# Kernel optimization log

Hardware: AMD Instinct MI355X
Metric: run time of the kernel (lower is better)

Reference implementation:

```python
import jax, jax.numpy as jnp
import numpy as np

D_MODEL = 1024
EXPAND = 2
D_INNER = EXPAND * D_MODEL      # 2048
D_STATE = 2
D_CONV = 4
DT_RANK = (D_MODEL + 15) // 16  # 64
BATCH, SEQ = 2, 4096
LN_EPS = 1e-5


def setup_inputs() -> dict:
    key = jax.random.key(0)
    ks = jax.random.split(key, 16)
    s = 0.02
    inp = {
        "x":       jax.random.normal(ks[0], (BATCH, SEQ, D_MODEL), jnp.float32),
        # Mamba params (torch Linear convention: W is [out, in])
        "w_in":    jax.random.normal(ks[1], (2 * D_INNER, D_MODEL), jnp.float32) * s,
        "conv_w":  jax.random.normal(ks[2], (D_INNER, 1, D_CONV), jnp.float32) * s,
        "conv_b":  jnp.zeros((D_INNER,), jnp.float32),
        "w_xproj": jax.random.normal(ks[3], (DT_RANK + 2 * D_STATE, D_INNER), jnp.float32) * s,
        "w_dt":    jax.random.normal(ks[4], (D_INNER, DT_RANK), jnp.float32) * s,
        "b_dt":    jax.random.normal(ks[5], (D_INNER,), jnp.float32) * s - 4.0,  # softplus -> small dt
        "a_log":   jnp.log(jnp.broadcast_to(jnp.arange(1, D_STATE + 1, dtype=jnp.float32), (D_INNER, D_STATE))),
        "d_skip":  jnp.ones((D_INNER,), jnp.float32),
        "w_out":   jax.random.normal(ks[6], (D_MODEL, D_INNER), jnp.float32) * s,
        # LayerNorms
        "ln1_g":   jnp.ones((D_MODEL,), jnp.float32),
        "ln1_b":   jnp.zeros((D_MODEL,), jnp.float32),
        "ln2_g":   jnp.ones((D_MODEL,), jnp.float32),
        "ln2_b":   jnp.zeros((D_MODEL,), jnp.float32),
        # FFN (Linear d->d, ReLU, Linear d->d; dropout inactive at eval)
        "ffn_w1":  jax.random.normal(ks[7], (D_MODEL, D_MODEL), jnp.float32) * s,
        "ffn_b1":  jnp.zeros((D_MODEL,), jnp.float32),
        "ffn_w2":  jax.random.normal(ks[8], (D_MODEL, D_MODEL), jnp.float32) * s,
        "ffn_b2":  jnp.zeros((D_MODEL,), jnp.float32),
    }
    return inp


def _ln(x, g, b):
    mu = x.mean(-1, keepdims=True)
    v = ((x - mu) ** 2).mean(-1, keepdims=True)
    return (x - mu) * jax.lax.rsqrt(v + LN_EPS) * g + b


def _mamba(x, w_in, conv_w, conv_b, w_xproj, w_dt, b_dt, a_log, d_skip, w_out):
    Bsz = x.shape[0]
    xz = x @ w_in.T                      # (B,L,2*D_INNER)
    xp, z = jnp.split(xz, 2, axis=-1)
    # depthwise causal conv over time
    xc = jnp.transpose(xp, (0, 2, 1))    # (B,D,L)
    xc = jax.lax.conv_general_dilated(
        xc, conv_w, window_strides=(1,), padding=[(D_CONV - 1, 0)],
        feature_group_count=D_INNER)
    xc = xc + conv_b[None, :, None]
    xp = jax.nn.silu(jnp.transpose(xc, (0, 2, 1)))   # (B,L,D)
    # input-dependent SSM params
    x_dbl = xp @ w_xproj.T               # (B,L,DT_RANK+2N)
    dt, Bm, Cm = jnp.split(x_dbl, [DT_RANK, DT_RANK + D_STATE], axis=-1)
    dt = jax.nn.softplus(dt @ w_dt.T + b_dt)          # (B,L,D)
    A = -jnp.exp(a_log)                  # (D,N)
    dA = jnp.exp(dt[..., None] * A)                  # (B,L,D,N)
    dBu = dt[..., None] * Bm[:, :, None, :] * xp[..., None]  # (B,L,D,N)

    def step(h, inp):
        da, dbu, c = inp                 # (B,D,N),(B,D,N),(B,N)
        h = da * h + dbu
        y = jnp.einsum('bdn,bn->bd', h, c)
        return h, y

    h0 = jnp.zeros((Bsz, D_INNER, D_STATE), x.dtype)
    _, ys = jax.lax.scan(step, h0, (jnp.swapaxes(dA, 0, 1),
                                    jnp.swapaxes(dBu, 0, 1),
                                    jnp.swapaxes(Cm, 0, 1)))
    y = jnp.swapaxes(ys, 0, 1)           # (B,L,D)
    y = (y + d_skip * xp) * jax.nn.silu(z)
    return y @ w_out.T                   # (B,L,d_model)


def reference(x, w_in, conv_w, conv_b, w_xproj, w_dt, b_dt, a_log, d_skip, w_out,
              ln1_g, ln1_b, ln2_g, ln2_b, ffn_w1, ffn_b1, ffn_w2, ffn_b2):
    h = x + _mamba(_ln(x, ln1_g, ln1_b), w_in, conv_w, conv_b, w_xproj,
                   w_dt, b_dt, a_log, d_skip, w_out)
    f = _ln(h, ln2_g, ln2_b)
    f = jax.nn.relu(f @ ffn_w1.T + ffn_b1) @ ffn_w2.T + ffn_b2
    return h + f
```

## Files before the change

kernel.cpp:

```cpp
#include <hip/hip_runtime.h>

typedef unsigned short u16;
typedef __bf16 bf16x8 __attribute__((ext_vector_type(8)));
typedef float f32x4 __attribute__((ext_vector_type(4)));
typedef float f32x2 __attribute__((ext_vector_type(2)));
typedef u16 u16x4 __attribute__((ext_vector_type(4)));
typedef u16 u16x8 __attribute__((ext_vector_type(8)));

#define SEQ   4096
#define DM    1024
#define DI    2048
#define NTOK  8192
#define NXP   68
#define DTR   64
#define NCH   4096
#define CHUNK 32
#define NCHK  128

__device__ __forceinline__ float bf2f(u16 v) {
  union { unsigned u; float f; } x; x.u = ((unsigned)v) << 16; return x.f;
}
__device__ __forceinline__ u16 f2bf(float f) {
  unsigned u = __float_as_uint(f);
  return (u16)((u + 0x7FFFu + ((u >> 16) & 1u)) >> 16);
}

__device__ __forceinline__ void g2l16(const u16* g, u16* l) {
  __builtin_amdgcn_global_load_lds(
      (const __attribute__((address_space(1))) unsigned int*)g,
      (__attribute__((address_space(3))) unsigned int*)l, 16, 0, 0);
}

#define SBAR0() __builtin_amdgcn_sched_barrier(0)

__global__ __launch_bounds__(256)
void detect_kernel(const u16* __restrict__ x, int* __restrict__ flag)
{
  __shared__ int tot;
  if (threadIdx.x == 0) tot = 0;
  __syncthreads();
  int cnt = 0;
  for (int i = threadIdx.x; i < 4096; i += 256) {
    const int e = (x[2 * i] >> 7) & 0xFF;
    if (e > 167) cnt++;
  }
  atomicAdd(&tot, cnt);
  __syncthreads();
  if (threadIdx.x == 0) flag[0] = (tot >= 8) ? 1 : 0;
}

#define NW0 4194304
#define NW1  139264
#define NW2  131072
#define NW3 2097152
#define NW4 1048576
#define NW5 1048576
#define NBB 4228
__global__ __launch_bounds__(256)
void convert_all(const float* __restrict__ s0, const float* __restrict__ s1,
                 const float* __restrict__ s2, const float* __restrict__ s3,
                 const float* __restrict__ s4, const float* __restrict__ s5,
                 u16* __restrict__ d0, u16* __restrict__ d1, u16* __restrict__ d2,
                 u16* __restrict__ d3, u16* __restrict__ d4, u16* __restrict__ d5,
                 const void* t0, const void* t1, const void* t2, const void* t3,
                 const void* t4, const void* t5, const void* t6, const void* t7,
                 const void* t8, const void* t9, const void* t10,
                 u16* __restrict__ dsm, const int* __restrict__ flag)
{
  if (blockIdx.x >= NBB) {
    const int i = (blockIdx.x - NBB) * 256 + threadIdx.x;
    if (i >= 24576) return;
    const void* src; int off; int dsti = i;
    if      (i < 8192)  { src = t0;  off = i;
                          dsti = (off & 3) * DI + (off >> 2); }
    else if (i < 10240) { src = t1;  off = i - 8192; }
    else if (i < 12288) { src = t2;  off = i - 10240; }
    else if (i < 16384) { src = t3;  off = i - 12288; }
    else if (i < 18432) { src = t4;  off = i - 16384; }
    else if (i < 19456) { src = t5;  off = i - 18432; }
    else if (i < 20480) { src = t6;  off = i - 19456; }
    else if (i < 21504) { src = t7;  off = i - 20480; }
    else if (i < 22528) { src = t8;  off = i - 21504; }
    else if (i < 23552) { src = t9;  off = i - 22528; }
    else                { src = t10; off = i - 23552; }
    dsm[dsti] = (*flag) ? f2bf(((const float*)src)[off]) : ((const u16*)src)[off];
    return;
  }
  if (*flag == 0) return;
  long e = ((long)blockIdx.x * 256 + threadIdx.x) * 8;
  const long c1 = NW0, c2 = c1 + NW1, c3 = c2 + NW2, c4 = c3 + NW3,
             c5 = c4 + NW4, c6 = c5 + NW5;
  if (e >= c6) return;
  const float* s; u16* d;
  if      (e < c1) { s = s0;          d = d0; }
  else if (e < c2) { s = s1; e -= c1; d = d1; }
  else if (e < c3) { s = s2; e -= c2; d = d2; }
  else if (e < c4) { s = s3; e -= c3; d = d3; }
  else if (e < c5) { s = s4; e -= c4; d = d4; }
  else             { s = s5; e -= c5; d = d5; }
  f32x4 a = *(const f32x4*)(s + e);
  f32x4 b = *(const f32x4*)(s + e + 4);
  u16x8 o;
#pragma unroll
  for (int k = 0; k < 4; ++k) { o[k] = f2bf(a[k]); o[4 + k] = f2bf(b[k]); }
  *(u16x8*)(d + e) = o;
}

template<int MODE>
__global__ __launch_bounds__(256)
void ln_kernel(const void* __restrict__ xin, const u16* __restrict__ gw,
               const u16* __restrict__ bw, u16* __restrict__ outp,
               const int* __restrict__ flag)
{
  const int tid = threadIdx.x;
  const int sub = tid >> 7;
  const int col0 = (tid & 127) * 8;
  const int row = blockIdx.x * 2 + sub;
  const bool isf32 = (MODE == 0) ? (*flag != 0) : false;
  float v[8];
  if (isf32) {
    const float* xf = (const float*)xin + (size_t)row * DM + col0;
    f32x4 a = *(const f32x4*)xf, b2 = *(const f32x4*)(xf + 4);
#pragma unroll
    for (int k = 0; k < 4; ++k) { v[k] = a[k]; v[4 + k] = b2[k]; }
  } else {
    u16x8 xb = *(const u16x8*)((const u16*)xin + (size_t)row * DM + col0);
#pragma unroll
    for (int k = 0; k < 8; ++k) v[k] = bf2f(xb[k]);
  }
  float s = 0.f, s2 = 0.f;
#pragma unroll
  for (int k = 0; k < 8; ++k) { s += v[k]; s2 += v[k] * v[k]; }
#pragma unroll
  for (int off = 32; off > 0; off >>= 1) {
    s  += __shfl_down(s,  off);
    s2 += __shfl_down(s2, off);
  }
  __shared__ float red[4], red2[4];
  __shared__ f32x2 stat[2];
  const int wv = tid >> 6;
  if ((tid & 63) == 0) { red[wv] = s; red2[wv] = s2; }
  __syncthreads();
  if ((tid & 127) == 0) {
    float ts = red[sub * 2] + red[sub * 2 + 1];
    float t2 = red2[sub * 2] + red2[sub * 2 + 1];
    float mu = ts * (1.f / DM);
    float var = t2 * (1.f / DM) - mu * mu;
    stat[sub] = f32x2{mu, rsqrtf(var + 1e-5f)};
  }
  __syncthreads();
  const float mu = stat[sub][0], rs = stat[sub][1];
  u16x8 gv = *(const u16x8*)(gw + col0), bv = *(const u16x8*)(bw + col0);
  u16x8 o;
#pragma unroll
  for (int k = 0; k < 8; ++k)
    o[k] = f2bf((v[k] - mu) * rs * bf2f(gv[k]) + bf2f(bv[k]));
  *(u16x8*)(outp + (size_t)row * DM + col0) = o;
}

template<int EPI, int LNBX>
__global__ __launch_bounds__(256, 2)
void gemm_kernel(const u16* __restrict__ A, const u16* __restrict__ Bc,
                 const u16* __restrict__ Braw,
                 int M, int N, int K,
                 const u16* __restrict__ bias, const u16* __restrict__ addbf,
                 const float* __restrict__ addf, const int* __restrict__ dtflag,
                 void* __restrict__ Cp, void* __restrict__ Cp2)
{
  __shared__ __align__(16) u16 sA[2][128 * 32];
  __shared__ __align__(16) u16 sB[2][128 * 32];
  const int fl = *dtflag;
  const u16* __restrict__ B = fl ? Bc : Braw;
  const int tid = threadIdx.x;
  const int b = blockIdx.x;
  const int xcd = b & 7;
  const int kk = b >> 3;
  const int bx = kk & ((1 << LNBX) - 1);
  const int by = xcd * 8 + (kk >> LNBX);
  const int m0 = by * 128;
  const int n0 = bx * 128;
  const int lane = tid & 63;
  const int wv = tid >> 6;
  const int wm = (wv & 1) * 64;
  const int wn = (wv >> 1) * 64;
  const int r = lane & 15;
  const int q = lane >> 4;
  const int rsw = (r >> 1) & 3;

  const int pr = lane >> 2;
  const int kc = (lane & 3) ^ ((pr >> 1) & 3);
  const int pk = kc * 8;
  u16* lA0[2] = { &sA[0][(wv * 2 + 0) * 512], &sA[1][(wv * 2 + 0) * 512] };
  u16* lA1[2] = { &sA[0][(wv * 2 + 1) * 512], &sA[1][(wv * 2 + 1) * 512] };
  u16* lB0[2] = { &sB[0][(wv * 2 + 0) * 512], &sB[1][(wv * 2 + 0) * 512] };
  u16* lB1[2] = { &sB[0][(wv * 2 + 1) * 512], &sB[1][(wv * 2 + 1) * 512] };
  const u16* gA0 = A + (size_t)(m0 + wv * 32 + pr) * K + pk;
  const u16* gA1 = gA0 + (size_t)16 * K;
  const u16* gB0 = B + (size_t)(n0 + wv * 32 + pr) * K + pk;
  const u16* gB1 = gB0 + (size_t)16 * K;

  f32x4 acc[4][4];
#pragma unroll
  for (int i = 0; i < 4; ++i)
#pragma unroll
    for (int j = 0; j < 4; ++j)
#pragma unroll
      for (int t = 0; t < 4; ++t) acc[i][j][t] = 0.f;

  g2l16(gA0, lA0[0]); g2l16(gA1, lA1[0]);
  g2l16(gB0, lB0[0]); g2l16(gB1, lB1[0]);

  const int nk = K >> 5;
  for (int kt = 0; kt < nk; ++kt) {
    const int cur = kt & 1;
    __syncthreads();
    bf16x8 af[4], bfr[4];
#pragma unroll
    for (int i = 0; i < 4; ++i)
      af[i] = *reinterpret_cast<const bf16x8*>(
          &sA[cur][(wm + i * 16 + r) * 32 + (q ^ rsw) * 8]);
#pragma unroll
    for (int j = 0; j < 4; ++j)
      bfr[j] = *reinterpret_cast<const bf16x8*>(
          &sB[cur][(wn + j * 16 + r) * 32 + (q ^ rsw) * 8]);
    if (kt + 1 < nk) {
      gA0 += 32; gA1 += 32; gB0 += 32; gB1 += 32;
      g2l16(gA0, lA0[cur ^ 1]); g2l16(gA1, lA1[cur ^ 1]);
      g2l16(gB0, lB0[cur ^ 1]); g2l16(gB1, lB1[cur ^ 1]);
    }
#pragma unroll
    for (int i = 0; i < 4; ++i)
#pragma unroll
      for (int j = 0; j < 4; ++j)
        acc[i][j] = __builtin_amdgcn_mfma_f32_16x16x32_bf16(af[i], bfr[j], acc[i][j], 0, 0, 0);
  }

  __syncthreads();
  float* ep = (wv < 2) ? ((float*)&sA[0][0] + wv * 2048)
                       : ((float*)&sB[0][0] + (wv - 2) * 2048);
  const int r2 = lane >> 2;
  const int ccol = ((lane & 3) ^ (r2 & 3)) * 16;

#pragma unroll
  for (int i = 0; i < 4; ++i) {
#pragma unroll
    for (int j = 0; j < 4; ++j)
#pragma unroll
      for (int t = 0; t < 4; ++t)
        ep[(q * 4 + t) * 68 + j * 16 + r] = acc[i][j][t];
    f32x4 w0 = *(const f32x4*)&ep[r2 * 68 + ccol + 0];
    f32x4 w1 = *(const f32x4*)&ep[r2 * 68 + ccol + 4];
    f32x4 w2 = *(const f32x4*)&ep[r2 * 68 + ccol + 8];
    f32x4 w3 = *(const f32x4*)&ep[r2 * 68 + ccol + 12];
    float vv[16];
#pragma unroll
    for (int k = 0; k < 4; ++k) {
      vv[k] = w0[k]; vv[4 + k] = w1[k]; vv[8 + k] = w2[k]; vv[12 + k] = w3[k];
    }
    const int row = m0 + wm + i * 16 + r2;
    const int colg = n0 + wn + ccol;
    const size_t idx = (size_t)row * N + colg;
    if (EPI == 2) {
      u16x8 b0 = *(const u16x8*)&bias[colg];
      u16x8 b1 = *(const u16x8*)&bias[colg + 8];
      u16x8 o0, o1;
#pragma unroll
      for (int k = 0; k < 8; ++k) {
        float v0 = vv[k] + bf2f(b0[k]);
        float v1 = vv[8 + k] + bf2f(b1[k]);
        v0 = (v0 > 15.f) ? v0 : __logf(1.f + __expf(v0));
        v1 = (v1 > 15.f) ? v1 : __logf(1.f + __expf(v1));
        o0[k] = f2bf(v0); o1[k] = f2bf(v1);
      }
      *(u16x8*)&((u16*)Cp)[idx] = o0;
      *(u16x8*)&((u16*)Cp)[idx + 8] = o1;
    } else if (EPI == 3) {
      float ax[16];
      if (fl) {
        f32x4 a0 = *(const f32x4*)&addf[idx];
        f32x4 a1 = *(const f32x4*)&addf[idx + 4];
        f32x4 a2 = *(const f32x4*)&addf[idx + 8];
        f32x4 a3 = *(const f32x4*)&addf[idx + 12];
#pragma unroll
        for (int k = 0; k < 4; ++k) {
          ax[k] = a0[k]; ax[4 + k] = a1[k]; ax[8 + k] = a2[k]; ax[12 + k] = a3[k];
        }
      } else {
        u16x8 a0 = *(const u16x8*)&addbf[idx];
        u16x8 a1 = *(const u16x8*)&addbf[idx + 8];
#pragma unroll
        for (int k = 0; k < 8; ++k) { ax[k] = bf2f(a0[k]); ax[8 + k] = bf2f(a1[k]); }
      }
      u16x8 o0, o1;
#pragma unroll
      for (int k = 0; k < 8; ++k) {
        o0[k] = f2bf(vv[k] + ax[k]); o1[k] = f2bf(vv[8 + k] + ax[8 + k]);
      }
      *(u16x8*)&((u16*)Cp)[idx] = o0;
      *(u16x8*)&((u16*)Cp)[idx + 8] = o1;
    } else if (EPI == 4) {
      u16x8 b0 = *(const u16x8*)&bias[colg];
      u16x8 b1 = *(const u16x8*)&bias[colg + 8];
      u16x8 o0, o1;
#pragma unroll
      for (int k = 0; k < 8; ++k) {
        o0[k] = f2bf(fmaxf(vv[k] + bf2f(b0[k]), 0.f));
        o1[k] = f2bf(fmaxf(vv[8 + k] + bf2f(b1[k]), 0.f));
      }
      *(u16x8*)&((u16*)Cp)[idx] = o0;
      *(u16x8*)&((u16*)Cp)[idx + 8] = o1;
    } else {
      u16x8 b0 = *(const u16x8*)&bias[colg];
      u16x8 b1 = *(const u16x8*)&bias[colg + 8];
      u16x8 a0 = *(const u16x8*)&addbf[idx];
      u16x8 a1 = *(const u16x8*)&addbf[idx + 8];
      float r0[8], r1[8];
#pragma unroll
      for (int k = 0; k < 8; ++k) {
        r0[k] = vv[k] + bf2f(b0[k]) + bf2f(a0[k]);
        r1[k] = vv[8 + k] + bf2f(b1[k]) + bf2f(a1[k]);
      }
      if (fl) {
        f32x4 f0, f1, f2, f3;
#pragma unroll
        for (int k = 0; k < 4; ++k) { f0[k] = r0[k]; f1[k] = r0[4 + k]; f2[k] = r1[k]; f3[k] = r1[4 + k]; }
        *(f32x4*)&((float*)Cp)[idx] = f0;
        *(f32x4*)&((float*)Cp)[idx + 4] = f1;
        *(f32x4*)&((float*)Cp)[idx + 8] = f2;
        *(f32x4*)&((float*)Cp)[idx + 12] = f3;
      } else {
        u16x8 o0, o1;
#pragma unroll
        for (int k = 0; k < 8; ++k) { o0[k] = f2bf(r0[k]); o1[k] = f2bf(r1[k]); }
        *(u16x8*)&((u16*)Cp)[idx] = o0;
        *(u16x8*)&((u16*)Cp)[idx + 8] = o1;
      }
    }
  }
}

template<int EPI, int LNBX>
__global__ __launch_bounds__(512, 2)
void gemm256_kernel(const u16* __restrict__ A, const u16* __restrict__ Bc,
                    const u16* __restrict__ Braw, int M, int N, int K,
                    const int* __restrict__ dtflag, void* __restrict__ Cp,
                    void* __restrict__ Cp2)
{
  __shared__ __align__(16) u16 sAB[2][2][2][128 * 64];
  (void)M;
  const int fl = *dtflag;
  const u16* __restrict__ B = fl ? Bc : Braw;
  const int tid = threadIdx.x;
  const int w = tid >> 6;
  const int lane = tid & 63;
  const int b = blockIdx.x;
  const int wg = (b & 7) * (gridDim.x >> 3) + (b >> 3);
  const int bx = wg & ((1 << LNBX) - 1);
  const int by = wg >> LNBX;
  const int m0 = by * 256;
  const int n0 = bx * 256;
  const int wm = w >> 2;
  const int wn = w & 3;
  const int r = lane & 15;
  const int q = lane >> 4;
  const int r7 = r & 7;
  const int srow = lane >> 3;
  const int schunk = ((lane & 7) ^ (srow & 7)) << 3;

  auto stageA = [&](int buf, int half, int kt) {
#pragma unroll
    for (int j = 0; j < 2; ++j) {
      u16* l = &sAB[buf][0][half][(w * 16 + j * 8) * 64];
      const u16* g = A + (size_t)(m0 + half * 128 + w * 16 + j * 8 + srow) * K
                       + (kt << 6) + schunk;
      g2l16(g, l);
    }
  };
  auto stageB = [&](int buf, int half, int kt) {
#pragma unroll
    for (int j = 0; j < 2; ++j) {
      u16* l = &sAB[buf][1][half][(w * 16 + j * 8) * 64];
      const u16* g = B + (size_t)(n0 + half * 128 + w * 16 + j * 8 + srow) * K
                       + (kt << 6) + schunk;
      g2l16(g, l);
    }
  };

  f32x4 acc[8][4];
#pragma unroll
  for (int i = 0; i < 8; ++i)
#pragma unroll
    for (int j = 0; j < 4; ++j)
#pragma unroll
      for (int t = 0; t < 4; ++t) acc[i][j][t] = 0.f;

  const int nk = K >> 6;
  stageA(0, 0, 0); stageA(0, 1, 0); stageB(0, 0, 0); stageB(0, 1, 0);
  if (nk > 1) { stageB(1, 0, 1); stageB(1, 1, 1); }
  if (nk > 1) asm volatile("s_waitcnt vmcnt(4)" ::: "memory");
  else        asm volatile("s_waitcnt vmcnt(0)" ::: "memory");
  SBAR0();
  __builtin_amdgcn_s_barrier();
  SBAR0();

  for (int kt = 0; kt < nk; ++kt) {
    const int c = kt & 1;
    const u16* bA = &sAB[c][0][wm][0];
    const u16* bB = &sAB[c][1][wn >> 1][0];
    const int rB = (wn & 1) * 64;
    bf16x8 af03[4][2], af47[4][2], b01[2][2], b23[2][2];

#pragma unroll
    for (int mf = 0; mf < 4; ++mf)
#pragma unroll
      for (int ks = 0; ks < 2; ++ks)
        af03[mf][ks] = *(const bf16x8*)&bA[(mf * 16 + r) * 64
                          + ((((ks << 2) + q) ^ r7) << 3)];
#pragma unroll
    for (int nf = 0; nf < 2; ++nf)
#pragma unroll
      for (int ks = 0; ks < 2; ++ks)
        b01[nf][ks] = *(const bf16x8*)&bB[(rB + nf * 16 + r) * 64
                          + ((((ks << 2) + q) ^ r7) << 3)];
    if (kt + 1 < nk) stageA(c ^ 1, 0, kt + 1);
    SBAR0(); __builtin_amdgcn_s_barrier();
    asm volatile("s_waitcnt lgkmcnt(0)" ::: "memory"); SBAR0();
    __builtin_amdgcn_s_setprio(1);
#pragma unroll
    for (int mf = 0; mf < 4; ++mf)
#pragma unroll
      for (int nf = 0; nf < 2; ++nf)
#pragma unroll
        for (int ks = 0; ks < 2; ++ks)
          acc[mf][nf] = __builtin_amdgcn_mfma_f32_16x16x32_bf16(
              af03[mf][ks], b01[nf][ks], acc[mf][nf], 0, 0, 0);
    __builtin_amdgcn_s_setprio(0);
    SBAR0(); __builtin_amdgcn_s_barrier(); SBAR0();

#pragma unroll
    for (int nf = 0; nf < 2; ++nf)
#pragma unroll
      for (int ks = 0; ks < 2; ++ks)
        b23[nf][ks] = *(const bf16x8*)&bB[(rB + (nf + 2) * 16 + r) * 64
                          + ((((ks << 2) + q) ^ r7) << 3)];
    if (kt + 1 < nk) stageA(c ^ 1, 1, kt + 1);
    SBAR0(); __builtin_amdgcn_s_barrier();
    asm volatile("s_waitcnt lgkmcnt(0)" ::: "memory"); SBAR0();
    __builtin_amdgcn_s_setprio(1);
#pragma unroll
    for (int mf = 0; mf < 4; ++mf)
#pragma unroll
      for (int nf = 0; nf < 2; ++nf)
#pragma unroll
        for (int ks = 0; ks < 2; ++ks)
          acc[mf][nf + 2] = __builtin_amdgcn_mfma_f32_16x16x32_bf16(
              af03[mf][ks], b23[nf][ks], acc[mf][nf + 2], 0, 0, 0);
    __builtin_amdgcn_s_setprio(0);
    SBAR0(); __builtin_amdgcn_s_barrier(); SBAR0();

#pragma unroll
    for (int mf = 0; mf < 4; ++mf)
#pragma unroll
      for (int ks = 0; ks < 2; ++ks)
        af47[mf][ks] = *(const bf16x8*)&bA[((mf + 4) * 16 + r) * 64
                          + ((((ks << 2) + q) ^ r7) << 3)];
    if (kt + 2 < nk) stageB(c, 0, kt + 2);
    SBAR0(); __builtin_amdgcn_s_barrier();
    asm volatile("s_waitcnt lgkmcnt(0)" ::: "memory"); SBAR0();
    __builtin_amdgcn_s_setprio(1);
#pragma unroll
    for (int mf = 0; mf < 4; ++mf)
#pragma unroll
      for (int nf = 0; nf < 2; ++nf)
#pragma unroll
        for (int ks = 0; ks < 2; ++ks)
          acc[mf + 4][nf + 2] = __builtin_amdgcn_mfma_f32_16x16x32_bf16(
              af47[mf][ks], b23[nf][ks], acc[mf + 4][nf + 2], 0, 0, 0);
    __builtin_amdgcn_s_setprio(0);
    SBAR0(); __builtin_amdgcn_s_barrier(); SBAR0();

    if (kt + 2 < nk) stageB(c, 1, kt + 2);
    SBAR0(); __builtin_amdgcn_s_barrier(); SBAR0();
    __builtin_amdgcn_s_setprio(1);
#pragma unroll
    for (int mf = 0; mf < 4; ++mf)
#pragma unroll
      for (int nf = 0; nf < 2; ++nf)
#pragma unroll
        for (int ks = 0; ks < 2; ++ks)
          acc[mf + 4][nf] = __builtin_amdgcn_mfma_f32_16x16x32_bf16(
              af47[mf][ks], b01[nf][ks], acc[mf + 4][nf], 0, 0, 0);
    __builtin_amdgcn_s_setprio(0);
    SBAR0();
    if (kt + 2 < nk) asm volatile("s_waitcnt vmcnt(4)" ::: "memory");
    else             asm volatile("s_waitcnt vmcnt(0)" ::: "memory");
    SBAR0();
    __builtin_amdgcn_s_barrier();
    SBAR0();
  }

  float* ep = (float*)&sAB[0][0][0][0] + w * 4096;
  const int r2 = lane >> 2;
  const int ccol = ((lane & 3) ^ (r2 & 3)) * 16;
  u16* C6 = (n0 < DI) ? (u16*)Cp : (u16*)Cp2;
  const int c6off = (n0 < DI) ? 0 : DI;
#pragma unroll
  for (int mf = 0; mf < 8; ++mf) {
#pragma unroll
    for (int nf = 0; nf < 4; ++nf)
#pragma unroll
      for (int t = 0; t < 4; ++t)
        ep[(q * 4 + t) * 68 + nf * 16 + r] = acc[mf][nf][t];
    f32x4 w0 = *(const f32x4*)&ep[r2 * 68 + ccol + 0];
    f32x4 w1 = *(const f32x4*)&ep[r2 * 68 + ccol + 4];
    f32x4 w2 = *(const f32x4*)&ep[r2 * 68 + ccol + 8];
    f32x4 w3 = *(const f32x4*)&ep[r2 * 68 + ccol + 12];
    u16x8 o0, o1;
#pragma unroll
    for (int k = 0; k < 4; ++k) {
      o0[k] = f2bf(w0[k]); o0[4 + k] = f2bf(w1[k]);
      o1[k] = f2bf(w2[k]); o1[4 + k] = f2bf(w3[k]);
    }
    const int row = m0 + wm * 128 + mf * 16 + r2;
    const int colg = n0 + wn * 64 + ccol;
    const size_t cb = (size_t)row * DI + (colg - c6off);
    *(u16x8*)&C6[cb] = o0;
    *(u16x8*)&C6[cb + 8] = o1;
  }
}

__global__ __launch_bounds__(256, 2)
void xproj_splitk(const u16* __restrict__ A, const u16* __restrict__ Bc,
                  const u16* __restrict__ Braw, const int* __restrict__ dtflag,
                  float* __restrict__ part)
{
  __shared__ __align__(16) u16 sA[2][128 * 32];
  __shared__ __align__(16) u16 sB[2][128 * 32];
  const int fl = *dtflag;
  const u16* __restrict__ B = fl ? Bc : Braw;
  const int tid = threadIdx.x;
  const int kz = blockIdx.x;
  const int m0 = blockIdx.y * 128;
  const int kbase = kz * 256;
  const int lane = tid & 63;
  const int wv = tid >> 6;
  const int wm = (wv & 1) * 64;
  const int wn = (wv >> 1) * 64;
  const int r = lane & 15;
  const int q = lane >> 4;
  const int rsw = (r >> 1) & 3;
  const int pr = lane >> 2;
  const int kc = (lane & 3) ^ ((pr >> 1) & 3);
  const int pk = kc * 8;

  u16* lA0[2] = { &sA[0][(wv * 2 + 0) * 512], &sA[1][(wv * 2 + 0) * 512] };
  u16* lA1[2] = { &sA[0][(wv * 2 + 1) * 512], &sA[1][(wv * 2 + 1) * 512] };
  u16* lB0[2] = { &sB[0][(wv * 2 + 0) * 512], &sB[1][(wv * 2 + 0) * 512] };
  u16* lB1[2] = { &sB[0][(wv * 2 + 1) * 512], &sB[1][(wv * 2 + 1) * 512] };
  int br0 = wv * 32 + pr;      if (br0 > 67) br0 = 67;
  int br1 = wv * 32 + 16 + pr; if (br1 > 67) br1 = 67;
  const u16* gA0 = A + (size_t)(m0 + wv * 32 + pr) * DI + kbase + pk;
  const u16* gA1 = gA0 + (size_t)16 * DI;
  const u16* gB0 = B + (size_t)br0 * DI + kbase + pk;
  const u16* gB1 = B + (size_t)br1 * DI + kbase + pk;

  f32x4 acc[4][4];
#pragma unroll
  for (int i = 0; i < 4; ++i)
#pragma unroll
    for (int j = 0; j < 4; ++j)
#pragma unroll
      for (int t = 0; t < 4; ++t) acc[i][j][t] = 0.f;

  g2l16(gA0, lA0[0]); g2l16(gA1, lA1[0]);
  g2l16(gB0, lB0[0]); g2l16(gB1, lB1[0]);

  for (int kt = 0; kt < 8; ++kt) {
    const int cur = kt & 1;
    __syncthreads();
    bf16x8 af[4], bfr[4];
#pragma unroll
    for (int i = 0; i < 4; ++i)
      af[i] = *reinterpret_cast<const bf16x8*>(
          &sA[cur][(wm + i * 16 + r) * 32 + (q ^ rsw) * 8]);
#pragma unroll
    for (int j = 0; j < 4; ++j)
      bfr[j] = *reinterpret_cast<const bf16x8*>(
          &sB[cur][(wn + j * 16 + r) * 32 + (q ^ rsw) * 8]);
    if (kt + 1 < 8) {
      gA0 += 32; gA1 += 32; gB0 += 32; gB1 += 32;
      g2l16(gA0, lA0[cur ^ 1]); g2l16(gA1, lA1[cur ^ 1]);
      g2l16(gB0, lB0[cur ^ 1]); g2l16(gB1, lB1[cur ^ 1]);
    }
#pragma unroll
    for (int i = 0; i < 4; ++i)
#pragma unroll
      for (int j = 0; j < 4; ++j)
        acc[i][j] = __builtin_amdgcn_mfma_f32_16x16x32_bf16(af[i], bfr[j], acc[i][j], 0, 0, 0);
  }

#pragma unroll
  for (int i = 0; i < 4; ++i)
#pragma unroll
    for (int j = 0; j < 4; ++j)
#pragma unroll
      for (int t = 0; t < 4; ++t) {
        const int row = m0 + wm + i * 16 + q * 4 + t;
        const int col = wn + j * 16 + r;
        if (col < NXP)
          part[((size_t)kz * NTOK + row) * NXP + col] = acc[i][j][t];
      }
}

__global__ __launch_bounds__(256)
void xreduce_kernel(const float* __restrict__ part, u16* __restrict__ dtraw,
                    float* __restrict__ bc)
{
  const int i = blockIdx.x * 256 + threadIdx.x;
  if (i >= NTOK * NXP) return;
  const int row = i / NXP, col = i - row * NXP;
  float s = 0.f;
#pragma unroll
  for (int z = 0; z < 8; ++z) s += part[(size_t)z * NTOK * NXP + i];
  if (col < DTR) dtraw[(size_t)row * DTR + col] = f2bf(s);
  else           bc[row * 4 + (col - DTR)] = s;
}

__global__ __launch_bounds__(256)
void conv_silu_kernel(const u16* __restrict__ xp, const u16* __restrict__ cwT,
                      const u16* __restrict__ cb, u16* __restrict__ u)
{
  const int token = blockIdx.x;
  const int t = token & (SEQ - 1);
  const int d0 = threadIdx.x * 8;
  const ptrdiff_t base = (ptrdiff_t)token * DI + d0;
  float acc[8];
  u16x8 cbv = *(const u16x8*)(cb + d0);
#pragma unroll
  for (int k = 0; k < 8; ++k) acc[k] = bf2f(cbv[k]);
#pragma unroll
  for (int j = 0; j < 4; ++j) {
    if (t - 3 + j >= 0) {
      u16x8 xv = *(const u16x8*)(xp + base + (ptrdiff_t)(j - 3) * DI);
      u16x8 wv = *(const u16x8*)(cwT + j * DI + d0);
#pragma unroll
      for (int k = 0; k < 8; ++k) acc[k] += bf2f(wv[k]) * bf2f(xv[k]);
    }
  }
  u16x8 o;
#pragma unroll
  for (int k = 0; k < 8; ++k) {
    const float sg = 1.f / (1.f + __expf(-acc[k]));
    o[k] = f2bf(acc[k] * sg);
  }
  *(u16x8*)(u + base) = o;
}

__global__ __launch_bounds__(256)
void scan_pass1(const u16* __restrict__ dtb, const u16* __restrict__ ub,
                const float* __restrict__ bc, const u16* __restrict__ a_log,
                float* __restrict__ S, float* __restrict__ hf0, float* __restrict__ hf1)
{
  const int g4 = blockIdx.x * 256 + threadIdx.x;
  const int chg = g4 & (NCH / 4 - 1);
  const int c = g4 >> 10;
  const int ch0 = chg * 4;
  const int b = ch0 >> 11;
  const int d0 = ch0 & (DI - 1);
  u16x8 av = *(const u16x8*)(a_log + d0 * 2);
  float A0[4], A1[4];
#pragma unroll
  for (int k = 0; k < 4; ++k) {
    A0[k] = -__expf(bf2f(av[2 * k]));
    A1[k] = -__expf(bf2f(av[2 * k + 1]));
  }
  float h0[4] = {0.f, 0.f, 0.f, 0.f}, h1[4] = {0.f, 0.f, 0.f, 0.f};
  float s[4] = {0.f, 0.f, 0.f, 0.f};
  const int row0 = b * SEQ + c * CHUNK;
  for (int i = 0; i < CHUNK; ++i) {
    const size_t row = row0 + i;
    u16x4 dtv = *(const u16x4*)(dtb + row * DI + d0);
    u16x4 uv  = *(const u16x4*)(ub + row * DI + d0);
    f32x2 Bv = *(const f32x2*)(bc + row * 4);
#pragma unroll
    for (int k = 0; k < 4; ++k) {
      const float dt = bf2f(dtv[k]);
      const float dtu = dt * bf2f(uv[k]);
      h0[k] = __expf(A0[k] * dt) * h0[k] + dtu * Bv[0];
      h1[k] = __expf(A1[k] * dt) * h1[k] + dtu * Bv[1];
      s[k] += dt;
    }
  }
  const size_t g0 = (size_t)c * NCH + ch0;
  *(f32x4*)(S + g0)   = f32x4{s[0], s[1], s[2], s[3]};
  *(f32x4*)(hf0 + g0) = f32x4{h0[0], h0[1], h0[2], h0[3]};
  *(f32x4*)(hf1 + g0) = f32x4{h1[0], h1[1], h1[2], h1[3]};
}

__global__ __launch_bounds__(256)
void scan_pass2(const float* __restrict__ S, const float* __restrict__ hf0,
                const float* __restrict__ hf1, const u16* __restrict__ a_log,
                float* __restrict__ hi0, float* __restrict__ hi1)
{
  const int ch = blockIdx.x * 256 + threadIdx.x;
  const int d = ch & (DI - 1);
  const float A0 = -__expf(bf2f(a_log[d * 2 + 0]));
  const float A1 = -__expf(bf2f(a_log[d * 2 + 1]));
  float h0 = 0.f, h1 = 0.f;
  size_t g = ch;
  float sv = S[g], f0 = hf0[g], f1 = hf1[g];
  for (int c = 0; c < NCHK; ++c) {
    float svn = 0.f, f0n = 0.f, f1n = 0.f;
    if (c + 1 < NCHK) {
      const size_t gn = g + NCH;
      svn = S[gn]; f0n = hf0[gn]; f1n = hf1[gn];
    }
    hi0[g] = h0; hi1[g] = h1;
    h0 = __expf(A0 * sv) * h0 + f0;
    h1 = __expf(A1 * sv) * h1 + f1;
    sv = svn; f0 = f0n; f1 = f1n;
    g += NCH;
  }
}

__global__ __launch_bounds__(256)
void scan_pass3(const u16* __restrict__ dtb, const u16* __restrict__ ub,
                const float* __restrict__ bc, const u16* __restrict__ zbuf,
                const u16* __restrict__ a_log, const u16* __restrict__ d_skip,
                const float* __restrict__ hi0, const float* __restrict__ hi1,
                u16* __restrict__ yb)
{
  const int g4 = blockIdx.x * 256 + threadIdx.x;
  const int chg = g4 & (NCH / 4 - 1);
  const int c = g4 >> 10;
  const int ch0 = chg * 4;
  const int b = ch0 >> 11;
  const int d0 = ch0 & (DI - 1);
  u16x8 av = *(const u16x8*)(a_log + d0 * 2);
  u16x4 dkv = *(const u16x4*)(d_skip + d0);
  float A0[4], A1[4], dsk[4];
#pragma unroll
  for (int k = 0; k < 4; ++k) {
    A0[k] = -__expf(bf2f(av[2 * k]));
    A1[k] = -__expf(bf2f(av[2 * k + 1]));
    dsk[k] = bf2f(dkv[k]);
  }
  const size_t g0 = (size_t)c * NCH + ch0;
  f32x4 h0v = *(const f32x4*)(hi0 + g0);
  f32x4 h1v = *(const f32x4*)(hi1 + g0);
  float h0[4], h1[4];
#pragma unroll
  for (int k = 0; k < 4; ++k) { h0[k] = h0v[k]; h1[k] = h1v[k]; }
  const int row0 = b * SEQ + c * CHUNK;
  for (int i = 0; i < CHUNK; ++i) {
    const size_t row = row0 + i;
    u16x4 dtv = *(const u16x4*)(dtb + row * DI + d0);
    u16x4 uv  = *(const u16x4*)(ub + row * DI + d0);
    u16x4 zv  = *(const u16x4*)(zbuf + row * DI + d0);
    f32x4 bcv = *(const f32x4*)(bc + row * 4);
    u16x4 o;
#pragma unroll
    for (int k = 0; k < 4; ++k) {
      const float dt = bf2f(dtv[k]);
      const float uu = bf2f(uv[k]);
      const float dtu = dt * uu;
      h0[k] = __expf(A0[k] * dt) * h0[k] + dtu * bcv[0];
      h1[k] = __expf(A1[k] * dt) * h1[k] + dtu * bcv[1];
      const float y = h0[k] * bcv[2] + h1[k] * bcv[3];
      const float z = bf2f(zv[k]);
      const float sz = z / (1.f + __expf(-z));
      o[k] = f2bf((y + dsk[k] * uu) * sz);
    }
    *(u16x4*)(yb + row * DI + d0) = o;
  }
}

extern "C" void kernel_launch(void* const* d_in, const int* in_sizes, int n_in,
                              void* d_out, int out_size, void* d_ws, size_t ws_size,
                              hipStream_t stream)
{
  const void* x       = d_in[0];
  const void* w_in    = d_in[1];
  const void* conv_w  = d_in[2];
  const void* conv_b  = d_in[3];
  const void* w_xproj = d_in[4];
  const void* w_dt    = d_in[5];
  const void* b_dt    = d_in[6];
  const void* a_log   = d_in[7];
  const void* d_skip  = d_in[8];
  const void* w_out   = d_in[9];
  const void* ln1_g   = d_in[10];
  const void* ln1_b   = d_in[11];
  const void* ln2_g   = d_in[12];
  const void* ln2_b   = d_in[13];
  const void* ffn_w1  = d_in[14];
  const void* ffn_b1  = d_in[15];
  const void* ffn_w2  = d_in[16];
  const void* ffn_b2  = d_in[17];
  char* ws = (char*)d_ws;

  const size_t o_flag  = 0;
  const size_t o_small = 256;
  const size_t o_cwout = o_small + 65536;
  const size_t o_cff1  = o_cwout + (size_t)DM * DI * 2;
  const size_t o_cff2  = o_cff1  + (size_t)DM * DM * 2;
  const size_t o_cxp   = o_cff2  + (size_t)DM * DM * 2;
  const size_t o_cwdt  = o_cxp   + (size_t)NXP * DI * 2;
  const size_t o_xn    = 9437184;
  const size_t o_xp    = o_xn + (size_t)NTOK * DM * 2;
  const size_t o_z     = o_xp + (size_t)NTOK * DI * 2;
  const size_t o_u     = o_z  + (size_t)NTOK * DI * 2;
  const size_t o_bc    = o_u  + (size_t)NTOK * DI * 2;
  const size_t SCN = (size_t)NCHK * NCH * 4;
  const size_t o_S   = o_xn + 0 * SCN;
  const size_t o_hf0 = o_xn + 1 * SCN;
  const size_t o_hf1 = o_xn + 2 * SCN;
  const size_t o_hi0 = o_xn + 3 * SCN;
  const size_t o_hi1 = o_xn + 4 * SCN;

  int*   flagp   = (int*)(ws + o_flag);
  u16*   csmall  = (u16*)(ws + o_small);
  u16*   c_cwT   = csmall +     0;
  u16*   c_convb = csmall +  8192;
  u16*   c_bdt   = csmall + 10240;
  u16*   c_alog  = csmall + 12288;
  u16*   c_dskip = csmall + 16384;
  u16*   c_ln1g  = csmall + 18432;
  u16*   c_ln1b  = csmall + 19456;
  u16*   c_ln2g  = csmall + 20480;
  u16*   c_ln2b  = csmall + 21504;
  u16*   c_fb1   = csmall + 22528;
  u16*   c_fb2   = csmall + 23552;
  u16*   c_wout  = (u16*)(ws + o_cwout);
  u16*   c_ff1   = (u16*)(ws + o_cff1);
  u16*   c_ff2   = (u16*)(ws + o_cff2);
  u16*   c_xproj = (u16*)(ws + o_cxp);
  u16*   c_wdt   = (u16*)(ws + o_cwdt);
  u16*   c_win   = (u16*)(ws + o_u);
  u16*   xn      = (u16*)(ws + o_xn);
  u16*   xp      = (u16*)(ws + o_xp);
  u16*   zb      = (u16*)(ws + o_z);
  u16*   u       = (u16*)(ws + o_u);
  float* part    = (float*)(ws + o_xp);
  u16*   dtraw   = (u16*)(ws + o_xn);
  u16*   dtb     = xp;
  u16*   yb      = xp;
  float* bc      = (float*)(ws + o_bc);
  float* S       = (float*)(ws + o_S);
  float* hf0     = (float*)(ws + o_hf0);
  float* hf1     = (float*)(ws + o_hf1);
  float* hi0     = (float*)(ws + o_hi0);
  float* hi1     = (float*)(ws + o_hi1);
  u16*   hb      = (u16*)(ws + o_z);
  u16*   hn      = (u16*)(ws + o_xn);
  u16*   f1      = (u16*)(ws + o_u);

  const dim3 blk(256);

  detect_kernel<<<1, blk, 0, stream>>>((const u16*)x, flagp);
  convert_all<<<NBB + 96, blk, 0, stream>>>(
      (const float*)w_in, (const float*)w_xproj, (const float*)w_dt,
      (const float*)w_out, (const float*)ffn_w1, (const float*)ffn_w2,
      c_win, c_xproj, c_wdt, c_wout, c_ff1, c_ff2,
      conv_w, conv_b, b_dt, a_log, d_skip,
      ln1_g, ln1_b, ln2_g, ln2_b, ffn_b1, ffn_b2,
      csmall, flagp);

  ln_kernel<0><<<NTOK / 2, blk, 0, stream>>>(x, c_ln1g, c_ln1b, xn, flagp);
  gemm256_kernel<6, 4><<<512, dim3(512), 0, stream>>>(
      xn, c_win, (const u16*)w_in, NTOK, 2 * DI, DM, flagp, xp, zb);
  conv_silu_kernel<<<NTOK, blk, 0, stream>>>(xp, c_cwT, c_convb, u);
  xproj_splitk<<<dim3(8, 64), blk, 0, stream>>>(u, c_xproj, (const u16*)w_xproj,
                                                flagp, part);
  xreduce_kernel<<<(NTOK * NXP + 255) / 256, blk, 0, stream>>>(part, dtraw, bc);
  gemm_kernel<2, 4><<<1024, blk, 0, stream>>>(dtraw, c_wdt, (const u16*)w_dt,
                                              NTOK, DI, DTR,
                                              c_bdt, nullptr, nullptr, flagp, dtb, nullptr);
  scan_pass1<<<NCHK * NCH / 4 / 256, blk, 0, stream>>>(dtb, u, bc, c_alog, S, hf0, hf1);
  scan_pass2<<<NCH / 256, blk, 0, stream>>>(S, hf0, hf1, c_alog, hi0, hi1);
  scan_pass3<<<NCHK * NCH / 4 / 256, blk, 0, stream>>>(dtb, u, bc, zb, c_alog, c_dskip,
                                                       hi0, hi1, yb);
  gemm_kernel<3, 3><<<512, blk, 0, stream>>>(yb, c_wout, (const u16*)w_out,
                                             NTOK, DM, DI,
                                             nullptr, (const u16*)x, (const float*)x,
                                             flagp, hb, nullptr);
  ln_kernel<1><<<NTOK / 2, blk, 0, stream>>>(hb, c_ln2g, c_ln2b, hn, flagp);
  gemm_kernel<4, 3><<<512, blk, 0, stream>>>(hn, c_ff1, (const u16*)ffn_w1,
                                             NTOK, DM, DM,
                                             c_fb1, nullptr, nullptr, flagp, f1, nullptr);
  gemm_kernel<5, 3><<<512, blk, 0, stream>>>(f1, c_ff2, (const u16*)ffn_w2,
                                             NTOK, DM, DM,
                                             c_fb2, hb, nullptr, flagp, d_out, nullptr);
}
```

Before: 463.4 us.

## Add double-buffered GEMM with split B-fragment loads for out-proj and FFN

Adds a new gemm_dp kernel with 128x128 tiles, double-buffered LDS for A and B, and a schedule that interleaves half-B fragment reads, global prefetch of the next K tiles, and MFMA bursts with raised wave priority. The out-projection and both FFN GEMMs now use it instead of gemm_kernel, and their epilogues move out of the old kernel. The aim is to hide global-load latency behind MFMA work in these three GEMMs, at the cost of more LDS use and a more delicate waitcnt and barrier schedule.

Measured after the change: 440.8 us. -4.9%, faster.

```diff
diff --git a/kernel.cpp b/kernel.cpp
--- a/kernel.cpp
+++ b/kernel.cpp
@@ -274,67 +274,6 @@
       }
       *(u16x8*)&((u16*)Cp)[idx] = o0;
       *(u16x8*)&((u16*)Cp)[idx + 8] = o1;
-    } else if (EPI == 3) {
-      float ax[16];
-      if (fl) {
-        f32x4 a0 = *(const f32x4*)&addf[idx];
-        f32x4 a1 = *(const f32x4*)&addf[idx + 4];
-        f32x4 a2 = *(const f32x4*)&addf[idx + 8];
-        f32x4 a3 = *(const f32x4*)&addf[idx + 12];
-#pragma unroll
-        for (int k = 0; k < 4; ++k) {
-          ax[k] = a0[k]; ax[4 + k] = a1[k]; ax[8 + k] = a2[k]; ax[12 + k] = a3[k];
-        }
-      } else {
-        u16x8 a0 = *(const u16x8*)&addbf[idx];
-        u16x8 a1 = *(const u16x8*)&addbf[idx + 8];
-#pragma unroll
-        for (int k = 0; k < 8; ++k) { ax[k] = bf2f(a0[k]); ax[8 + k] = bf2f(a1[k]); }
-      }
-      u16x8 o0, o1;
-#pragma unroll
-      for (int k = 0; k < 8; ++k) {
-        o0[k] = f2bf(vv[k] + ax[k]); o1[k] = f2bf(vv[8 + k] + ax[8 + k]);
-      }
-      *(u16x8*)&((u16*)Cp)[idx] = o0;
-      *(u16x8*)&((u16*)Cp)[idx + 8] = o1;
-    } else if (EPI == 4) {
-      u16x8 b0 = *(const u16x8*)&bias[colg];
-      u16x8 b1 = *(const u16x8*)&bias[colg + 8];
-      u16x8 o0, o1;
-#pragma unroll
-      for (int k = 0; k < 8; ++k) {
-        o0[k] = f2bf(fmaxf(vv[k] + bf2f(b0[k]), 0.f));
-        o1[k] = f2bf(fmaxf(vv[8 + k] + bf2f(b1[k]), 0.f));
-      }
-      *(u16x8*)&((u16*)Cp)[idx] = o0;
-      *(u16x8*)&((u16*)Cp)[idx + 8] = o1;
-    } else {
-      u16x8 b0 = *(const u16x8*)&bias[colg];
-      u16x8 b1 = *(const u16x8*)&bias[colg + 8];
-      u16x8 a0 = *(const u16x8*)&addbf[idx];
-      u16x8 a1 = *(const u16x8*)&addbf[idx + 8];
-      float r0[8], r1[8];
-#pragma unroll
-      for (int k = 0; k < 8; ++k) {
-        r0[k] = vv[k] + bf2f(b0[k]) + bf2f(a0[k]);
-        r1[k] = vv[8 + k] + bf2f(b1[k]) + bf2f(a1[k]);
-      }
-      if (fl) {
-        f32x4 f0, f1, f2, f3;
-#pragma unroll
-        for (int k = 0; k < 4; ++k) { f0[k] = r0[k]; f1[k] = r0[4 + k]; f2[k] = r1[k]; f3[k] = r1[4 + k]; }
-        *(f32x4*)&((float*)Cp)[idx] = f0;
-        *(f32x4*)&((float*)Cp)[idx + 4] = f1;
-        *(f32x4*)&((float*)Cp)[idx + 8] = f2;
-        *(f32x4*)&((float*)Cp)[idx + 12] = f3;
-      } else {
-        u16x8 o0, o1;
-#pragma unroll
-        for (int k = 0; k < 8; ++k) { o0[k] = f2bf(r0[k]); o1[k] = f2bf(r1[k]); }
-        *(u16x8*)&((u16*)Cp)[idx] = o0;
-        *(u16x8*)&((u16*)Cp)[idx + 8] = o1;
-      }
     }
   }
 }
@@ -526,6 +465,214 @@
     const size_t cb = (size_t)row * DI + (colg - c6off);
     *(u16x8*)&C6[cb] = o0;
     *(u16x8*)&C6[cb + 8] = o1;
+  }
+}
+
+template<int EPI, int LNBX>
+__global__ __launch_bounds__(256, 2)
+void gemm_dp(const u16* __restrict__ A, const u16* __restrict__ Bc,
+             const u16* __restrict__ Braw, int M, int N, int K,
+             const u16* __restrict__ bias, const u16* __restrict__ addbf,
+             const float* __restrict__ addf, const int* __restrict__ dtflag,
+             void* __restrict__ Cp, void* __restrict__ Cp2)
+{
+  __shared__ __align__(16) u16 sA[2][128 * 64];
+  __shared__ __align__(16) u16 sB[2][128 * 64];
+  (void)M;
+  const int fl = *dtflag;
+  const u16* __restrict__ B = fl ? Bc : Braw;
+  const int tid = threadIdx.x;
+  const int lane = tid & 63;
+  const int w = tid >> 6;
+  const int b = blockIdx.x;
+  const int wg = (b & 7) * ((int)gridDim.x >> 3) + (b >> 3);
+  const int bx = wg & ((1 << LNBX) - 1);
+  const int by = wg >> LNBX;
+  const int m0 = by * 128;
+  const int n0 = bx * 128;
+  const int wm = (w & 1) * 64;
+  const int wn = (w >> 1) * 64;
+  const int r = lane & 15;
+  const int q = lane >> 4;
+  const int r7 = lane & 7;
+  const int srow = lane >> 3;
+  const int schunk = ((lane & 7) ^ (srow & 7)) << 3;
+
+  auto stage = [&](u16* dst, const u16* gbase, int ld) {
+#pragma unroll
+    for (int j = 0; j < 4; ++j) {
+      u16* l = dst + ((j * 4 + w) * 8) * 64;
+      const u16* g = gbase + (size_t)((j * 4 + w) * 8 + srow) * ld + schunk;
+      g2l16(g, l);
+    }
+  };
+  const u16* gA = A + (size_t)m0 * K;
+  const u16* gB = B + (size_t)n0 * K;
+
+  f32x4 acc[4][4];
+#pragma unroll
+  for (int i = 0; i < 4; ++i)
+#pragma unroll
+    for (int j = 0; j < 4; ++j)
+#pragma unroll
+      for (int t = 0; t < 4; ++t) acc[i][j][t] = 0.f;
+
+  const int nk = K >> 6;
+  stage(&sA[0][0], gA, K);
+  stage(&sB[0][0], gB, K);
+  if (nk > 1) {
+    stage(&sA[1][0], gA + 64, K);
+    asm volatile("s_waitcnt vmcnt(4)" ::: "memory");
+  } else {
+    asm volatile("s_waitcnt vmcnt(0)" ::: "memory");
+  }
+  SBAR0();
+  __builtin_amdgcn_s_barrier();
+  SBAR0();
+
+  for (int kt = 0; kt < nk; ++kt) {
+    const int c = kt & 1;
+    bf16x8 af[4][2], b01[2][2], b23[2][2];
+
+#pragma unroll
+    for (int mf = 0; mf < 4; ++mf)
+#pragma unroll
+      for (int ks = 0; ks < 2; ++ks)
+        af[mf][ks] = *(const bf16x8*)&sA[c][(wm + mf * 16 + r) * 64
+                        + ((((ks << 2) + q) ^ r7) << 3)];
+#pragma unroll
+    for (int nf = 0; nf < 2; ++nf)
+#pragma unroll
+      for (int ks = 0; ks < 2; ++ks)
+        b01[nf][ks] = *(const bf16x8*)&sB[c][(wn + nf * 16 + r) * 64
+                        + ((((ks << 2) + q) ^ r7) << 3)];
+    if (kt + 1 < nk) stage(&sB[c ^ 1][0], gB + (size_t)(kt + 1) * 64, K);
+    SBAR0();
+    __builtin_amdgcn_s_barrier();
+    SBAR0();
+    __builtin_amdgcn_s_setprio(1);
+#pragma unroll
+    for (int mf = 0; mf < 4; ++mf)
+#pragma unroll
+      for (int nf = 0; nf < 2; ++nf)
+#pragma unroll
+        for (int ks = 0; ks < 2; ++ks)
+          acc[mf][nf] = __builtin_amdgcn_mfma_f32_16x16x32_bf16(
+              af[mf][ks], b01[nf][ks], acc[mf][nf], 0, 0, 0);
+    __builtin_amdgcn_s_setprio(0);
+    SBAR0();
+
+#pragma unroll
+    for (int nf = 0; nf < 2; ++nf)
+#pragma unroll
+      for (int ks = 0; ks < 2; ++ks)
+        b23[nf][ks] = *(const bf16x8*)&sB[c][(wn + (nf + 2) * 16 + r) * 64
+                        + ((((ks << 2) + q) ^ r7) << 3)];
+    if (kt + 2 < nk) stage(&sA[c][0], gA + (size_t)(kt + 2) * 64, K);
+    if (kt + 2 < nk) asm volatile("s_waitcnt vmcnt(4)" ::: "memory");
+    else             asm volatile("s_waitcnt vmcnt(0)" ::: "memory");
+    SBAR0();
+    __builtin_amdgcn_s_barrier();
+    SBAR0();
+    __builtin_amdgcn_s_setprio(1);
+#pragma unroll
+    for (int mf = 0; mf < 4; ++mf)
+#pragma unroll
+      for (int nf = 0; nf < 2; ++nf)
+#pragma unroll
+        for (int ks = 0; ks < 2; ++ks)
+          acc[mf][nf + 2] = __builtin_amdgcn_mfma_f32_16x16x32_bf16(
+              af[mf][ks], b23[nf][ks], acc[mf][nf + 2], 0, 0, 0);
+    __builtin_amdgcn_s_setprio(0);
+    SBAR0();
+  }
+
+  __syncthreads();
+  float* ep = (w < 2) ? ((float*)&sA[0][0] + w * 2048)
+                      : ((float*)&sB[0][0] + (w - 2) * 2048);
+  const int r2 = lane >> 2;
+  const int ccol = ((lane & 3) ^ (r2 & 3)) * 16;
+#pragma unroll
+  for (int i = 0; i < 4; ++i) {
+#pragma unroll
+    for (int j = 0; j < 4; ++j)
+#pragma unroll
+      for (int t = 0; t < 4; ++t)
+        ep[(q * 4 + t) * 68 + j * 16 + r] = acc[i][j][t];
+    f32x4 w0 = *(const f32x4*)&ep[r2 * 68 + ccol + 0];
+    f32x4 w1 = *(const f32x4*)&ep[r2 * 68 + ccol + 4];
+    f32x4 w2 = *(const f32x4*)&ep[r2 * 68 + ccol + 8];
+    f32x4 w3 = *(const f32x4*)&ep[r2 * 68 + ccol + 12];
+    float vv[16];
+#pragma unroll
+    for (int k = 0; k < 4; ++k) {
+      vv[k] = w0[k]; vv[4 + k] = w1[k]; vv[8 + k] = w2[k]; vv[12 + k] = w3[k];
+    }
+    const int row = m0 + wm + i * 16 + r2;
+    const int colg = n0 + wn + ccol;
+    const size_t idx = (size_t)row * N + colg;
+    if (EPI == 3) {
+      float ax[16];
+      if (fl) {
+        f32x4 a0 = *(const f32x4*)&addf[idx];
+        f32x4 a1 = *(const f32x4*)&addf[idx + 4];
+        f32x4 a2 = *(const f32x4*)&addf[idx + 8];
+        f32x4 a3 = *(const f32x4*)&addf[idx + 12];
+#pragma unroll
+        for (int k = 0; k < 4; ++k) {
+          ax[k] = a0[k]; ax[4 + k] = a1[k]; ax[8 + k] = a2[k]; ax[12 + k] = a3[k];
+        }
+      } else {
+        u16x8 a0 = *(const u16x8*)&addbf[idx];
+        u16x8 a1 = *(const u16x8*)&addbf[idx + 8];
+#pragma unroll
+        for (int k = 0; k < 8; ++k) { ax[k] = bf2f(a0[k]); ax[8 + k] = bf2f(a1[k]); }
+      }
+      u16x8 o0, o1;
+#pragma unroll
+      for (int k = 0; k < 8; ++k) {
+        o0[k] = f2bf(vv[k] + ax[k]); o1[k] = f2bf(vv[8 + k] + ax[8 + k]);
+      }
+      *(u16x8*)&((u16*)Cp)[idx] = o0;
+      *(u16x8*)&((u16*)Cp)[idx + 8] = o1;
+    } else if (EPI == 4) {
+      u16x8 b0 = *(const u16x8*)&bias[colg];
+      u16x8 b1 = *(const u16x8*)&bias[colg + 8];
+      u16x8 o0, o1;
+#pragma unroll
+      for (int k = 0; k < 8; ++k) {
+        o0[k] = f2bf(fmaxf(vv[k] + bf2f(b0[k]), 0.f));
+        o1[k] = f2bf(fmaxf(vv[8 + k] + bf2f(b1[k]), 0.f));
+      }
+      *(u16x8*)&((u16*)Cp)[idx] = o0;
+      *(u16x8*)&((u16*)Cp)[idx + 8] = o1;
+    } else {
+      u16x8 b0 = *(const u16x8*)&bias[colg];
+      u16x8 b1 = *(const u16x8*)&bias[colg + 8];
+      u16x8 a0 = *(const u16x8*)&addbf[idx];
+      u16x8 a1 = *(const u16x8*)&addbf[idx + 8];
+      float r0[8], r1[8];
+#pragma unroll
+      for (int k = 0; k < 8; ++k) {
+        r0[k] = vv[k] + bf2f(b0[k]) + bf2f(a0[k]);
+        r1[k] = vv[8 + k] + bf2f(b1[k]) + bf2f(a1[k]);
+      }
+      if (fl) {
+        f32x4 f0, f1, f2, f3;
+#pragma unroll
+        for (int k = 0; k < 4; ++k) { f0[k] = r0[k]; f1[k] = r0[4 + k]; f2[k] = r1[k]; f3[k] = r1[4 + k]; }
+        *(f32x4*)&((float*)Cp)[idx] = f0;
+        *(f32x4*)&((float*)Cp)[idx + 4] = f1;
+        *(f32x4*)&((float*)Cp)[idx + 8] = f2;
+        *(f32x4*)&((float*)Cp)[idx + 12] = f3;
+      } else {
+        u16x8 o0, o1;
+#pragma unroll
+        for (int k = 0; k < 8; ++k) { o0[k] = f2bf(r0[k]); o1[k] = f2bf(r1[k]); }
+        *(u16x8*)&((u16*)Cp)[idx] = o0;
+        *(u16x8*)&((u16*)Cp)[idx + 8] = o1;
+      }
+    }
   }
 }
 
@@ -880,15 +1027,15 @@
   scan_pass2<<<NCH / 256, blk, 0, stream>>>(S, hf0, hf1, c_alog, hi0, hi1);
   scan_pass3<<<NCHK * NCH / 4 / 256, blk, 0, stream>>>(dtb, u, bc, zb, c_alog, c_dskip,
                                                        hi0, hi1, yb);
-  gemm_kernel<3, 3><<<512, blk, 0, stream>>>(yb, c_wout, (const u16*)w_out,
-                                             NTOK, DM, DI,
-                                             nullptr, (const u16*)x, (const float*)x,
-                                             flagp, hb, nullptr);
+  gemm_dp<3, 3><<<512, blk, 0, stream>>>(yb, c_wout, (const u16*)w_out,
+                                         NTOK, DM, DI,
+                                         nullptr, (const u16*)x, (const float*)x,
+                                         flagp, hb, nullptr);
   ln_kernel<1><<<NTOK / 2, blk, 0, stream>>>(hb, c_ln2g, c_ln2b, hn, flagp);
-  gemm_kernel<4, 3><<<512, blk, 0, stream>>>(hn, c_ff1, (const u16*)ffn_w1,
-                                             NTOK, DM, DM,
-                                             c_fb1, nullptr, nullptr, flagp, f1, nullptr);
-  gemm_kernel<5, 3><<<512, blk, 0, stream>>>(f1, c_ff2, (const u16*)ffn_w2,
-                                             NTOK, DM, DM,
-                                             c_fb2, hb, nullptr, flagp, d_out, nullptr);
-}
+  gemm_dp<4, 3><<<512, blk, 0, stream>>>(hn, c_ff1, (const u16*)ffn_w1,
+                                         NTOK, DM, DM,
+                                         c_fb1, nullptr, nullptr, flagp, f1, nullptr);
+  gemm_dp<5, 3><<<512, blk, 0, stream>>>(f1, c_ff2, (const u16*)ffn_w2,
+                                         NTOK, DM, DM,
+                                         c_fb2, hb, nullptr, flagp, d_out, nullptr);
+}
```
